# Optimization experiments

Measured on AMD Instinct MI355X. Metric: run time of the kernel, lower is better.

Reference implementation:

```python
import jax, jax.numpy as jnp
import numpy as np

# Static geometry constants (match input_specs / init_kwargs)
B, NP, C_IN = 16, 4096, 64          # clouds, points per cloud, feature dim
RATIO, RAD = 0.25, 0.2
M = int(RATIO * NP)
HID, OUT = 64, 128


def setup_inputs() -> dict:
    key = jax.random.key(0)
    ks = jax.random.split(key, 8)
    point = jax.random.uniform(ks[0], (B * NP, 3), dtype=jnp.float32)
    xyz = jax.random.normal(ks[1], (B * NP, C_IN), dtype=jnp.float32)
    batch = jnp.arange(B * NP, dtype=jnp.int32) // NP  # contiguous equal-size clouds
    s = 0.05
    W1 = jax.random.normal(ks[2], (C_IN + 3, HID), dtype=jnp.float32) * s
    b1 = jnp.zeros((HID,), jnp.float32)
    W2 = jax.random.normal(ks[3], (HID, HID), dtype=jnp.float32) * s
    b2 = jnp.zeros((HID,), jnp.float32)
    W3 = jax.random.normal(ks[4], (HID, OUT), dtype=jnp.float32) * s
    b3 = jnp.zeros((OUT,), jnp.float32)
    return {"xyz": xyz, "point": point, "batch": batch, "num_samples": 64,
            "W1": W1, "b1": b1, "W2": W2, "b2": b2, "W3": W3, "b3": b3}


def _fps(p):
    """Farthest point sampling on one cloud p:[NP,3] -> [M] local indices (start at 0)."""
    d0 = jnp.sum((p - p[0]) ** 2, axis=-1)
    def step(d, _):
        nxt = jnp.argmax(d).astype(jnp.int32)
        d = jnp.minimum(d, jnp.sum((p - p[nxt]) ** 2, axis=-1))
        return d, nxt
    _, rest = jax.lax.scan(step, d0, None, length=M - 1)
    return jnp.concatenate([jnp.zeros((1,), jnp.int32), rest])


def reference(xyz, point, batch, num_samples, W1, b1, W2, b2, W3, b3):
    K = int(num_samples)
    pos = point.reshape(B, NP, 3)
    feat = xyz.reshape(B, NP, C_IN)

    # fps(point, batch, ratio)
    idx = jax.vmap(_fps)(pos)                                      # [B,M]
    centers = jnp.take_along_axis(pos, idx[..., None], axis=1)      # [B,M,3]

    # radius(point, point[idx], rad, max_num_neighbors=K): take K nearest in-ball
    d2 = jnp.sum((centers[:, :, None, :] - pos[:, None, :, :]) ** 2, axis=-1)  # [B,M,NP]
    valid = d2 < RAD * RAD
    sel = jnp.where(valid, d2, jnp.inf)
    _, nidx = jax.lax.top_k(-jax.lax.stop_gradient(sel), K)         # [B,M,K]
    mask = jnp.take_along_axis(valid, nidx, axis=2)                 # [B,M,K]

    # PointConv: msg = local_nn(cat([x_j, pos_j - pos_i])), aggr = max
    bi = jnp.arange(B)[:, None, None]
    pos_j = pos[bi, nidx]                                           # [B,M,K,3]
    feat_j = feat[bi, nidx]                                         # [B,M,K,C]
    msg = jnp.concatenate([feat_j, pos_j - centers[:, :, None, :]], axis=-1)
    h = jax.nn.relu(msg @ W1 + b1)
    h = jax.nn.relu(h @ W2 + b2)
    h = jax.nn.relu(h @ W3 + b3)                                    # [B,M,K,OUT]
    h = jnp.where(mask[..., None], h, -jnp.inf)
    out = jnp.max(h, axis=2).reshape(B * M, OUT)

    idx_g = (idx + jnp.arange(B, dtype=jnp.int32)[:, None] * NP).reshape(-1)
    return out, centers.reshape(B * M, 3), batch[idx_g]
```

## Files before the change

kernel.cpp:

```cpp
#include <hip/hip_runtime.h>
#include <cstdint>

#define NB 16
#define NP 4096
#define MC 1024
#define KNN 64
#define CIN 64
#define HID 64
#define OUTD 128

typedef __attribute__((ext_vector_type(8))) short bf16x8;
typedef __attribute__((ext_vector_type(4))) float f32x4;
typedef __attribute__((ext_vector_type(2))) float f32x2;
typedef unsigned long long ull;
typedef unsigned short ushort_t;

#define F32_INF __int_as_float(0x7f800000)
#define WSENT 0xFFFFFFFFu

#define BAR_LGKM() asm volatile("s_waitcnt lgkmcnt(0)\n\ts_barrier" ::: "memory")

__device__ __forceinline__ float dist2e(float ax, float ay, float az,
                                        float bx, float by, float bz) {
  float dx = __fsub_rn(ax, bx);
  float dy = __fsub_rn(ay, by);
  float dz = __fsub_rn(az, bz);
  return __fadd_rn(__fadd_rn(__fmul_rn(dx, dx), __fmul_rn(dy, dy)), __fmul_rn(dz, dz));
}

__device__ __forceinline__ ushort_t f2bf(float f) {
  unsigned u = __float_as_uint(f);
  unsigned r = (u + 0x7FFFu + ((u >> 16) & 1u)) >> 16;
  return (ushort_t)r;
}

template <int CTRL>
__device__ __forceinline__ ull kshift(ull k) {
  int lo = (int)(unsigned)(k & 0xffffffffULL);
  int hi = (int)(unsigned)(k >> 32);
  lo = __builtin_amdgcn_update_dpp(lo, lo, CTRL, 0xf, 0xf, false);
  hi = __builtin_amdgcn_update_dpp(hi, hi, CTRL, 0xf, 0xf, false);
  return ((ull)(unsigned)hi << 32) | (ull)(unsigned)lo;
}
template <int CTRL>
__device__ __forceinline__ ull kred(ull k) {
  ull o = kshift<CTRL>(k);
  return (o > k) ? o : k;
}

__device__ __forceinline__ void wfrag_entry(const float* __restrict__ W,
                                            ushort_t* __restrict__ out,
                                            int e, int KS, int K, int N) {
  int lane = e & 63, t2 = e >> 6;
  int ks = t2 % KS, nt = t2 / KS;
  int n = nt * 16 + (lane & 15);
  int kb = ks * 32 + ((lane >> 4) & 3) * 8;
#pragma unroll
  for (int j = 0; j < 8; ++j) {
    int k = kb + j;
    float v = (k < K) ? W[(size_t)k * N + n] : 0.f;
    out[(size_t)e * 8 + j] = f2bf(v);
  }
}

__global__ void init_widx(unsigned* __restrict__ widx) {
  int i = blockIdx.x * 256 + threadIdx.x;
  if (i < NB * MC) widx[i] = WSENT;
}

__global__ __launch_bounds__(256) void mega_kernel(
    const float* __restrict__ point, const float* __restrict__ xyz,
    const float* __restrict__ W1, const float* __restrict__ W2, const float* __restrict__ W3,
    const float* __restrict__ b1, const float* __restrict__ b2, const float* __restrict__ b3,
    unsigned* __restrict__ widx,
    float* __restrict__ out, float* __restrict__ cent_out, float* __restrict__ batch_out) {
#pragma clang fp contract(off)
  __shared__ char __attribute__((aligned(16))) smem[74752];
  const int blk = blockIdx.x;
  const int t = threadIdx.x;

  if (blk < NB) {
    const int b = blk;
    const int lane = t & 63, wid = t >> 6;
    float4* pts = (float4*)smem;
    ull* kbuf = (ull*)(smem + 65536);
    int* whist = (int*)(smem + 65600);
    const float* p = point + (size_t)b * NP * 3;
    for (int i = t; i < NP; i += 256) {
      float4 v; v.x = p[3 * i]; v.y = p[3 * i + 1]; v.z = p[3 * i + 2]; v.w = 0.f;
      pts[i] = v;
    }
    if (t == 0) {
      whist[0] = 0;
      __hip_atomic_store(widx + (size_t)b * MC, 0u, __ATOMIC_RELAXED, __HIP_MEMORY_SCOPE_AGENT);
    }
    __syncthreads();
    f32x2 qx2[8], qy2[8], qz2[8], d2v[8];
#pragma unroll
    for (int k = 0; k < 8; ++k) {
      float4 v0 = pts[t * 16 + 2 * k];
      float4 v1 = pts[t * 16 + 2 * k + 1];
      qx2[k].x = v0.x; qx2[k].y = v1.x;
      qy2[k].x = v0.y; qy2[k].y = v1.y;
      qz2[k].x = v0.z; qz2[k].y = v1.z;
      d2v[k].x = F32_INF; d2v[k].y = F32_INF;
    }
    int w = 0;
    for (int it = 1; it < MC; ++it) {
      float4 wp = pts[w];
      f32x2 wxx; wxx.x = wp.x; wxx.y = wp.x;
      f32x2 wyy; wyy.x = wp.y; wyy.y = wp.y;
      f32x2 wzz; wzz.x = wp.z; wzz.y = wp.z;
      float bd = -1.0f; int br = 0;
#pragma unroll
      for (int k = 0; k < 8; ++k) {
        f32x2 dx = qx2[k] - wxx;
        f32x2 dy = qy2[k] - wyy;
        f32x2 dz = qz2[k] - wzz;
        f32x2 nd = (dx * dx + dy * dy) + dz * dz;
        f32x2 dv;
        dv.x = fminf(d2v[k].x, nd.x);
        dv.y = fminf(d2v[k].y, nd.y);
        d2v[k] = dv;
        bool p1 = dv.y > dv.x;
        float pd = p1 ? dv.y : dv.x;
        int pr = 2 * k + (p1 ? 1 : 0);
        if (pd > bd) { bd = pd; br = pr; }
      }
      unsigned gi = (unsigned)(t * 16 + br);
      ull key = ((ull)__float_as_uint(bd) << 32) | (ull)(unsigned)~gi;
      key = kred<0x111>(key);
      key = kred<0x112>(key);
      key = kred<0x114>(key);
      key = kred<0x118>(key);
      key = kred<0x142>(key);
      key = kred<0x143>(key);
      const int par = it & 1;
      if (lane == 63) kbuf[par * 4 + wid] = key;
      BAR_LGKM();
      ull k0 = kbuf[par * 4 + 0], k1 = kbuf[par * 4 + 1];
      ull k2 = kbuf[par * 4 + 2], k3 = kbuf[par * 4 + 3];
      ull ka = (k0 > k1) ? k0 : k1;
      ull kb = (k2 > k3) ? k2 : k3;
      ull km = (ka > kb) ? ka : kb;
      w = (int)~(unsigned)(km & 0xffffffffULL);
      if (t == 0) {
        whist[it] = w;
        __hip_atomic_store(widx + (size_t)b * MC + it, (unsigned)w,
                           __ATOMIC_RELAXED, __HIP_MEMORY_SCOPE_AGENT);
      }
    }
    __syncthreads();
    for (int s = t; s < MC; s += 256) {
      int wi = whist[s];
      float4 wp = pts[wi];
      size_t o = (size_t)b * MC + s;
      cent_out[3*o] = wp.x; cent_out[3*o+1] = wp.y; cent_out[3*o+2] = wp.z;
      batch_out[o] = (float)b;
    }
    return;
  }

  const int wv = t >> 6, lane = t & 63;
  const int quad = lane >> 4, col16 = lane & 15;
  ushort_t* w1L = (ushort_t*)smem;
  ushort_t* w2L = (ushort_t*)(smem + 12288);
  ushort_t* w3L = (ushort_t*)(smem + 20480);
  for (int e = t; e < 4 * 3 * 64; e += 256) wfrag_entry(W1, w1L, e, 3, CIN + 3, HID);
  for (int e = t; e < 4 * 2 * 64; e += 256) wfrag_entry(W2, w2L, e, 2, HID, HID);
  for (int e = t; e < 8 * 2 * 64; e += 256) wfrag_entry(W3, w3L, e, 2, HID, OUTD);
  __syncthreads();

  char* base = smem + 36864 + wv * 9472;
  float* ld = (float*)base;
  int* li = (int*)(base + 2048);
  ushort_t* hb = (ushort_t*)base;
  int* nsel = (int*)(base + 9216);
  const float R2 = (float)(0.2 * 0.2);
  const int gwave = (blk - NB) * 4 + wv;

  for (int r = gwave; r < NB * MC; r += 960) {
    const int s = r >> 4, b = r & 15;
    const int c = b * MC + s;
    const size_t bbase = (size_t)b * NP;
    unsigned wpub = 0;
    if (lane == 0) {
      wpub = __hip_atomic_load(widx + c, __ATOMIC_RELAXED, __HIP_MEMORY_SCOPE_AGENT);
      while (wpub == WSENT) {
        __builtin_amdgcn_s_sleep(32);
        wpub = __hip_atomic_load(widx + c, __ATOMIC_RELAXED, __HIP_MEMORY_SCOPE_AGENT);
      }
    }
    const int wc = __shfl((int)wpub, 0);
    const float cx = point[(bbase + wc) * 3];
    const float cy = point[(bbase + wc) * 3 + 1];
    const float cz = point[(bbase + wc) * 3 + 2];

    const float* p = point + bbase * 3;
    int cnt = 0;
    for (int sb = 0; sb < NP / 64; ++sb) {
      int j = sb * 64 + lane;
      float d2 = dist2e(cx, cy, cz, p[3*j], p[3*j+1], p[3*j+2]);
      bool v = d2 < R2;
      ull m = __ballot(v);
      if (v) {
        int pos = cnt + __popcll(m & ((1ull << lane) - 1ull));
        if (pos < 512) { ld[pos] = d2; li[pos] = j; }
      }
      cnt += __popcll(m);
    }
    if (cnt > 512) cnt = 512;
    asm volatile("s_waitcnt lgkmcnt(0)" ::: "memory");
    if (cnt <= KNN) {
      nsel[lane] = (lane < cnt) ? li[lane] : 0;
    } else {
      unsigned ob[8]; int oi[8];
#pragma unroll
      for (int rr = 0; rr < 8; ++rr) {
        int s2 = lane + rr * 64;
        if (s2 < cnt) { ob[rr] = __float_as_uint(ld[s2]); oi[rr] = li[s2]; }
        else { ob[rr] = 0xFFFFFFFFu; oi[rr] = 0; }
      }
      unsigned L = 0u, H = 0x3D23D70Au;
      while (L < H) {
        unsigned mid = (L + H) >> 1;
        int cle = 0;
#pragma unroll
        for (int rr = 0; rr < 8; ++rr) cle += (int)__popcll(__ballot(ob[rr] <= mid));
        if (cle >= KNN) H = mid; else L = mid + 1;
      }
      const unsigned tau = H;
      int c_lt = 0;
#pragma unroll
      for (int rr = 0; rr < 8; ++rr) c_lt += (int)__popcll(__ballot(ob[rr] < tau));
      const int need = KNN - c_lt;
      const ull below = (1ull << lane) - 1ull;
      int outpos = 0, eqc = 0;
#pragma unroll
      for (int rr = 0; rr < 8; ++rr) {
        ull meq = __ballot(ob[rr] == tau);
        int eqrank = eqc + (int)__popcll(meq & below);
        bool sel = (ob[rr] < tau) || ((ob[rr] == tau) && (eqrank < need));
        ull msel = __ballot(sel);
        if (sel) {
          int posn = outpos + (int)__popcll(msel & below);
          nsel[posn] = oi[rr];
        }
        outpos += (int)__popcll(msel);
        eqc += (int)__popcll(meq);
      }
    }
    const int nv = (cnt < KNN) ? cnt : KNN;
    asm volatile("s_waitcnt lgkmcnt(0)" ::: "memory");
    const int jg = nsel[lane];

    const float* pp = point + (bbase + jg) * 3;
    const float dxx = pp[0] - cx, dyy = pp[1] - cy, dzz = pp[2] - cz;

    bf16x8 a1[4][2];
    bf16x8 a2[4];
#pragma unroll
    for (int mt = 0; mt < 4; ++mt) {
      int srcl = mt * 16 + col16;
      int jmt = __shfl(jg, srcl);
      const float* xr = xyz + (bbase + (size_t)jmt) * CIN + quad * 8;
      float4 f0 = *(const float4*)(xr);
      float4 f1 = *(const float4*)(xr + 4);
      float4 f2 = *(const float4*)(xr + 32);
      float4 f3 = *(const float4*)(xr + 36);
      bf16x8 v0, v1;
      v0[0] = (short)f2bf(f0.x); v0[1] = (short)f2bf(f0.y);
      v0[2] = (short)f2bf(f0.z); v0[3] = (short)f2bf(f0.w);
      v0[4] = (short)f2bf(f1.x); v0[5] = (short)f2bf(f1.y);
      v0[6] = (short)f2bf(f1.z); v0[7] = (short)f2bf(f1.w);
      v1[0] = (short)f2bf(f2.x); v1[1] = (short)f2bf(f2.y);
      v1[2] = (short)f2bf(f2.z); v1[3] = (short)f2bf(f2.w);
      v1[4] = (short)f2bf(f3.x); v1[5] = (short)f2bf(f3.y);
      v1[6] = (short)f2bf(f3.z); v1[7] = (short)f2bf(f3.w);
      a1[mt][0] = v0;
      a1[mt][1] = v1;
      float ddx = __shfl(dxx, srcl), ddy = __shfl(dyy, srcl), ddz = __shfl(dzz, srcl);
      bf16x8 t2 = {0, 0, 0, 0, 0, 0, 0, 0};
      if (quad == 0) {
        t2[0] = (short)f2bf(ddx); t2[1] = (short)f2bf(ddy); t2[2] = (short)f2bf(ddz);
      }
      a2[mt] = t2;
    }

    bf16x8 bw1[4][3];
#pragma unroll
    for (int nt = 0; nt < 4; ++nt)
#pragma unroll
      for (int ks = 0; ks < 3; ++ks)
        bw1[nt][ks] = *(const bf16x8*)(w1L + ((size_t)(nt * 3 + ks) * 64 + lane) * 8);
    f32x4 acc1[4][4];
#pragma unroll
    for (int nt = 0; nt < 4; ++nt) {
      float bv = b1[nt * 16 + col16];
#pragma unroll
      for (int mt = 0; mt < 4; ++mt) { f32x4 v = {bv, bv, bv, bv}; acc1[mt][nt] = v; }
    }
#pragma unroll
    for (int mt = 0; mt < 4; ++mt)
#pragma unroll
      for (int nt = 0; nt < 4; ++nt) {
        acc1[mt][nt] = __builtin_amdgcn_mfma_f32_16x16x32_bf16(a1[mt][0], bw1[nt][0], acc1[mt][nt], 0, 0, 0);
        acc1[mt][nt] = __builtin_amdgcn_mfma_f32_16x16x32_bf16(a1[mt][1], bw1[nt][1], acc1[mt][nt], 0, 0, 0);
        acc1[mt][nt] = __builtin_amdgcn_mfma_f32_16x16x32_bf16(a2[mt],    bw1[nt][2], acc1[mt][nt], 0, 0, 0);
      }
#pragma unroll
    for (int mt = 0; mt < 4; ++mt)
#pragma unroll
      for (int nt = 0; nt < 4; ++nt)
#pragma unroll
        for (int reg = 0; reg < 4; ++reg) {
          int row = quad * 4 + reg + mt * 16;
          hb[row * 72 + col16 + nt * 16] = f2bf(fmaxf(acc1[mt][nt][reg], 0.f));
        }

    bf16x8 a21[4][2];
#pragma unroll
    for (int mt = 0; mt < 4; ++mt)
#pragma unroll
      for (int ks = 0; ks < 2; ++ks)
        a21[mt][ks] = *(const bf16x8*)(hb + (col16 + mt * 16) * 72 + ks * 32 + quad * 8);
    bf16x8 bw2[4][2];
#pragma unroll
    for (int nt = 0; nt < 4; ++nt)
#pragma unroll
      for (int ks = 0; ks < 2; ++ks)
        bw2[nt][ks] = *(const bf16x8*)(w2L + ((size_t)(nt * 2 + ks) * 64 + lane) * 8);
    f32x4 acc2[4][4];
#pragma unroll
    for (int nt = 0; nt < 4; ++nt) {
      float bv = b2[nt * 16 + col16];
#pragma unroll
      for (int mt = 0; mt < 4; ++mt) { f32x4 v = {bv, bv, bv, bv}; acc2[mt][nt] = v; }
    }
#pragma unroll
    for (int mt = 0; mt < 4; ++mt)
#pragma unroll
      for (int nt = 0; nt < 4; ++nt) {
        acc2[mt][nt] = __builtin_amdgcn_mfma_f32_16x16x32_bf16(a21[mt][0], bw2[nt][0], acc2[mt][nt], 0, 0, 0);
        acc2[mt][nt] = __builtin_amdgcn_mfma_f32_16x16x32_bf16(a21[mt][1], bw2[nt][1], acc2[mt][nt], 0, 0, 0);
      }
#pragma unroll
    for (int mt = 0; mt < 4; ++mt)
#pragma unroll
      for (int nt = 0; nt < 4; ++nt)
#pragma unroll
        for (int reg = 0; reg < 4; ++reg) {
          int row = quad * 4 + reg + mt * 16;
          hb[row * 72 + col16 + nt * 16] = f2bf(fmaxf(acc2[mt][nt][reg], 0.f));
        }

    bf16x8 a3[4][2];
#pragma unroll
    for (int mt = 0; mt < 4; ++mt)
#pragma unroll
      for (int ks = 0; ks < 2; ++ks)
        a3[mt][ks] = *(const bf16x8*)(hb + (col16 + mt * 16) * 72 + ks * 32 + quad * 8);
#pragma unroll
    for (int pass = 0; pass < 2; ++pass) {
      bf16x8 bw3[4][2];
#pragma unroll
      for (int nt = 0; nt < 4; ++nt)
#pragma unroll
        for (int ks = 0; ks < 2; ++ks)
          bw3[nt][ks] = *(const bf16x8*)(w3L + ((size_t)((pass * 4 + nt) * 2 + ks) * 64 + lane) * 8);
      f32x4 acc3[4][4];
#pragma unroll
      for (int nt = 0; nt < 4; ++nt) {
        float bv = b3[pass * 64 + nt * 16 + col16];
#pragma unroll
        for (int mt = 0; mt < 4; ++mt) { f32x4 v = {bv, bv, bv, bv}; acc3[mt][nt] = v; }
      }
#pragma unroll
      for (int mt = 0; mt < 4; ++mt)
#pragma unroll
        for (int nt = 0; nt < 4; ++nt) {
          acc3[mt][nt] = __builtin_amdgcn_mfma_f32_16x16x32_bf16(a3[mt][0], bw3[nt][0], acc3[mt][nt], 0, 0, 0);
          acc3[mt][nt] = __builtin_amdgcn_mfma_f32_16x16x32_bf16(a3[mt][1], bw3[nt][1], acc3[mt][nt], 0, 0, 0);
        }
#pragma unroll
      for (int nt = 0; nt < 4; ++nt) {
        float m = -1.0e30f;
#pragma unroll
        for (int mt = 0; mt < 4; ++mt)
#pragma unroll
          for (int reg = 0; reg < 4; ++reg) {
            int row = quad * 4 + reg + mt * 16;
            float v = fmaxf(acc3[mt][nt][reg], 0.f);
            m = fmaxf(m, (row < nv) ? v : -1.0e30f);
          }
        m = fmaxf(m, __shfl_xor(m, 16));
        m = fmaxf(m, __shfl_xor(m, 32));
        if (quad == 0)
          out[(size_t)c * OUTD + pass * 64 + nt * 16 + col16] = m;
      }
    }
  }
}

extern "C" void kernel_launch(void* const* d_in, const int* in_sizes, int n_in,
                              void* d_out, int out_size, void* d_ws, size_t ws_size,
                              hipStream_t stream) {
  const float* xyz   = (const float*)d_in[0];
  const float* point = (const float*)d_in[1];
  const float* W1 = (const float*)d_in[4];
  const float* b1 = (const float*)d_in[5];
  const float* W2 = (const float*)d_in[6];
  const float* b2 = (const float*)d_in[7];
  const float* W3 = (const float*)d_in[8];
  const float* b3 = (const float*)d_in[9];

  float* out       = (float*)d_out;
  float* cent_out  = out + (size_t)NB * MC * OUTD;
  float* batch_out = cent_out + (size_t)NB * MC * 3;

  unsigned* widx = (unsigned*)d_ws;

  init_widx<<<64, 256, 0, stream>>>(widx);
  mega_kernel<<<256, 256, 0, stream>>>(point, xyz, W1, W2, W3, b1, b2, b3,
                                       widx, out, cent_out, batch_out);
}
```

Measured before the change: 759.1 us.

## Precompute bf16 weight fragments in init kernel and shrink LDS to raise occupancy

Moves the bf16 MFMA weight-fragment conversion from every worker block into the init kernel, which writes the fragments to workspace. Worker waves now load B fragments from global memory instead of LDS. The FPS block stores points as SoA instead of float4, which shrinks shared memory from about 73 KB to 52 KB so more blocks can be resident per CU. The worker grid grows from 240 to 720 blocks to use that occupancy. The cost is that weight reads move from LDS to global/L2 in every iteration, and more concurrent waves contend with the FPS blocks.

```diff
diff --git a/kernel.cpp b/kernel.cpp
--- a/kernel.cpp
+++ b/kernel.cpp
@@ -17,6 +17,8 @@
 
 #define F32_INF __int_as_float(0x7f800000)
 #define WSENT 0xFFFFFFFFu
+#define NWORK 720
+#define NWAVES (NWORK * 4)
 
 #define BAR_LGKM() asm volatile("s_waitcnt lgkmcnt(0)\n\ts_barrier" ::: "memory")
 
@@ -63,32 +65,48 @@
   }
 }
 
-__global__ void init_widx(unsigned* __restrict__ widx) {
-  int i = blockIdx.x * 256 + threadIdx.x;
-  if (i < NB * MC) widx[i] = WSENT;
+__global__ void init_kernel(unsigned* __restrict__ widx,
+                            const float* __restrict__ W1, const float* __restrict__ W2,
+                            const float* __restrict__ W3,
+                            ushort_t* __restrict__ w1f, ushort_t* __restrict__ w2f,
+                            ushort_t* __restrict__ w3f) {
+  const int blk = blockIdx.x, t = threadIdx.x;
+  if (blk < 64) {
+    int i = blk * 256 + t;
+    widx[i] = WSENT;
+  } else if (blk == 64) {
+    for (int e = t; e < 4 * 3 * 64; e += 256) wfrag_entry(W1, w1f, e, 3, CIN + 3, HID);
+  } else if (blk == 65) {
+    for (int e = t; e < 4 * 2 * 64; e += 256) wfrag_entry(W2, w2f, e, 2, HID, HID);
+  } else {
+    for (int e = (blk - 66) * 512 + t; e < (blk - 65) * 512; e += 256)
+      wfrag_entry(W3, w3f, e, 2, HID, OUTD);
+  }
 }
 
 __global__ __launch_bounds__(256) void mega_kernel(
     const float* __restrict__ point, const float* __restrict__ xyz,
-    const float* __restrict__ W1, const float* __restrict__ W2, const float* __restrict__ W3,
+    const ushort_t* __restrict__ w1f, const ushort_t* __restrict__ w2f,
+    const ushort_t* __restrict__ w3f,
     const float* __restrict__ b1, const float* __restrict__ b2, const float* __restrict__ b3,
     unsigned* __restrict__ widx,
     float* __restrict__ out, float* __restrict__ cent_out, float* __restrict__ batch_out) {
 #pragma clang fp contract(off)
-  __shared__ char __attribute__((aligned(16))) smem[74752];
+  __shared__ char __attribute__((aligned(16))) smem[53312];
   const int blk = blockIdx.x;
   const int t = threadIdx.x;
 
   if (blk < NB) {
     const int b = blk;
     const int lane = t & 63, wid = t >> 6;
-    float4* pts = (float4*)smem;
-    ull* kbuf = (ull*)(smem + 65536);
-    int* whist = (int*)(smem + 65600);
+    float* px = (float*)smem;
+    float* py = (float*)(smem + 16384);
+    float* pz = (float*)(smem + 32768);
+    ull* kbuf = (ull*)(smem + 49152);
+    int* whist = (int*)(smem + 49216);
     const float* p = point + (size_t)b * NP * 3;
     for (int i = t; i < NP; i += 256) {
-      float4 v; v.x = p[3 * i]; v.y = p[3 * i + 1]; v.z = p[3 * i + 2]; v.w = 0.f;
-      pts[i] = v;
+      px[i] = p[3 * i]; py[i] = p[3 * i + 1]; pz[i] = p[3 * i + 2];
     }
     if (t == 0) {
       whist[0] = 0;
@@ -98,19 +116,18 @@
     f32x2 qx2[8], qy2[8], qz2[8], d2v[8];
 #pragma unroll
     for (int k = 0; k < 8; ++k) {
-      float4 v0 = pts[t * 16 + 2 * k];
-      float4 v1 = pts[t * 16 + 2 * k + 1];
-      qx2[k].x = v0.x; qx2[k].y = v1.x;
-      qy2[k].x = v0.y; qy2[k].y = v1.y;
-      qz2[k].x = v0.z; qz2[k].y = v1.z;
+      int i0 = t * 16 + 2 * k, i1 = t * 16 + 2 * k + 1;
+      qx2[k].x = px[i0]; qx2[k].y = px[i1];
+      qy2[k].x = py[i0]; qy2[k].y = py[i1];
+      qz2[k].x = pz[i0]; qz2[k].y = pz[i1];
       d2v[k].x = F32_INF; d2v[k].y = F32_INF;
     }
     int w = 0;
     for (int it = 1; it < MC; ++it) {
-      float4 wp = pts[w];
-      f32x2 wxx; wxx.x = wp.x; wxx.y = wp.x;
-      f32x2 wyy; wyy.x = wp.y; wyy.y = wp.y;
-      f32x2 wzz; wzz.x = wp.z; wzz.y = wp.z;
+      float wx = px[w], wy = py[w], wz = pz[w];
+      f32x2 wxx; wxx.x = wx; wxx.y = wx;
+      f32x2 wyy; wyy.x = wy; wyy.y = wy;
+      f32x2 wzz; wzz.x = wz; wzz.y = wz;
       float bd = -1.0f; int br = 0;
 #pragma unroll
       for (int k = 0; k < 8; ++k) {
@@ -153,9 +170,9 @@
     __syncthreads();
     for (int s = t; s < MC; s += 256) {
       int wi = whist[s];
-      float4 wp = pts[wi];
+      float wx = px[wi], wy = py[wi], wz = pz[wi];
       size_t o = (size_t)b * MC + s;
-      cent_out[3*o] = wp.x; cent_out[3*o+1] = wp.y; cent_out[3*o+2] = wp.z;
+      cent_out[3*o] = wx; cent_out[3*o+1] = wy; cent_out[3*o+2] = wz;
       batch_out[o] = (float)b;
     }
     return;
@@ -163,15 +180,7 @@
 
   const int wv = t >> 6, lane = t & 63;
   const int quad = lane >> 4, col16 = lane & 15;
-  ushort_t* w1L = (ushort_t*)smem;
-  ushort_t* w2L = (ushort_t*)(smem + 12288);
-  ushort_t* w3L = (ushort_t*)(smem + 20480);
-  for (int e = t; e < 4 * 3 * 64; e += 256) wfrag_entry(W1, w1L, e, 3, CIN + 3, HID);
-  for (int e = t; e < 4 * 2 * 64; e += 256) wfrag_entry(W2, w2L, e, 2, HID, HID);
-  for (int e = t; e < 8 * 2 * 64; e += 256) wfrag_entry(W3, w3L, e, 2, HID, OUTD);
-  __syncthreads();
-
-  char* base = smem + 36864 + wv * 9472;
+  char* base = smem + wv * 9472;
   float* ld = (float*)base;
   int* li = (int*)(base + 2048);
   ushort_t* hb = (ushort_t*)base;
@@ -179,7 +188,7 @@
   const float R2 = (float)(0.2 * 0.2);
   const int gwave = (blk - NB) * 4 + wv;
 
-  for (int r = gwave; r < NB * MC; r += 960) {
+  for (int r = gwave; r < NB * MC; r += NWAVES) {
     const int s = r >> 4, b = r & 15;
     const int c = b * MC + s;
     const size_t bbase = (size_t)b * NP;
@@ -292,7 +301,7 @@
     for (int nt = 0; nt < 4; ++nt)
 #pragma unroll
       for (int ks = 0; ks < 3; ++ks)
-        bw1[nt][ks] = *(const bf16x8*)(w1L + ((size_t)(nt * 3 + ks) * 64 + lane) * 8);
+        bw1[nt][ks] = *(const bf16x8*)(w1f + ((size_t)(nt * 3 + ks) * 64 + lane) * 8);
     f32x4 acc1[4][4];
 #pragma unroll
     for (int nt = 0; nt < 4; ++nt) {
@@ -329,7 +338,7 @@
     for (int nt = 0; nt < 4; ++nt)
 #pragma unroll
       for (int ks = 0; ks < 2; ++ks)
-        bw2[nt][ks] = *(const bf16x8*)(w2L + ((size_t)(nt * 2 + ks) * 64 + lane) * 8);
+        bw2[nt][ks] = *(const bf16x8*)(w2f + ((size_t)(nt * 2 + ks) * 64 + lane) * 8);
     f32x4 acc2[4][4];
 #pragma unroll
     for (int nt = 0; nt < 4; ++nt) {
@@ -367,7 +376,7 @@
       for (int nt = 0; nt < 4; ++nt)
 #pragma unroll
         for (int ks = 0; ks < 2; ++ks)
-          bw3[nt][ks] = *(const bf16x8*)(w3L + ((size_t)((pass * 4 + nt) * 2 + ks) * 64 + lane) * 8);
+          bw3[nt][ks] = *(const bf16x8*)(w3f + ((size_t)((pass * 4 + nt) * 2 + ks) * 64 + lane) * 8);
       f32x4 acc3[4][4];
 #pragma unroll
       for (int nt = 0; nt < 4; ++nt) {
@@ -418,9 +427,14 @@
   float* cent_out  = out + (size_t)NB * MC * OUTD;
   float* batch_out = cent_out + (size_t)NB * MC * 3;
 
-  unsigned* widx = (unsigned*)d_ws;
-
-  init_widx<<<64, 256, 0, stream>>>(widx);
-  mega_kernel<<<256, 256, 0, stream>>>(point, xyz, W1, W2, W3, b1, b2, b3,
-                                       widx, out, cent_out, batch_out);
-}
+  char* ws = (char*)d_ws;
+  unsigned* widx  = (unsigned*)ws;
+  ushort_t* w1f   = (ushort_t*)(ws + 65536);
+  ushort_t* w2f   = (ushort_t*)(ws + 65536 + 12288);
+  ushort_t* w3f   = (ushort_t*)(ws + 65536 + 20480);
+
+  init_kernel<<<68, 256, 0, stream>>>(widx, W1, W2, W3, w1f, w2f, w3f);
+  mega_kernel<<<NB + NWORK, 256, 0, stream>>>(point, xyz, w1f, w2f, w3f,
+                                              b1, b2, b3, widx,
+                                              out, cent_out, batch_out);
+}
```

After: 956.3 us. 26.0% more time.
